# Performance work log

Hardware: AMD Instinct MI355X
Metric: run time of the kernel (lower is better)

The kernel has to match this reference:

```python
import jax, jax.numpy as jnp
import numpy as np

N, D_IN, D_OUT, E = 16384, 2048, 2048, 8


def setup_inputs() -> dict:
    key = jax.random.key(0)
    k1, k2, k3, k4 = jax.random.split(key, 4)
    x = jax.random.normal(k1, (N, D_IN), dtype=jnp.float32)
    idxs = jax.random.randint(k2, (N,), 0, E, dtype=jnp.int64)
    # nn.Linear params: weight [out, in], bias [out]; stacked over experts.
    W = jax.random.normal(k3, (E, D_OUT, D_IN), dtype=jnp.float32) * (1.0 / np.sqrt(D_IN))
    b = jax.random.normal(k4, (E, D_OUT), dtype=jnp.float32) * 0.01
    return {"x": x, "idxs": idxs, "W": W, "b": b}


def reference(x, idxs, W, b):
    # Hard-routed MoE: each token goes to exactly one expert's Linear, then ReLU.
    # Loop over the small fixed expert count; each iteration is one dense GEMM
    # over all tokens, combined with a per-token routing mask (equivalent math
    # to the original masked gather/scatter since every token matches exactly
    # one expert id in [0, E)).
    n_experts = W.shape[0]
    y = jnp.zeros((x.shape[0], W.shape[1]), dtype=x.dtype)
    for e in range(n_experts):
        mask = (idxs == e)[:, None]  # [N, 1]
        y_e = x @ W[e].T + b[e]      # [N, out]
        y = jnp.where(mask, y_e, y)
    return jax.nn.relu(y)
```

## Files before the change

### kernel.cpp

```cpp
#include <hip/hip_runtime.h>
#include <stdint.h>

#define N_TOK 16384
#define D_IN  2048
#define D_OUT 2048
#define NEXP  8

#define BM 256
#define BN 256
#define BK 32
#define NKT (D_IN / BK)

typedef __attribute__((ext_vector_type(8))) short bf16x8;
typedef __attribute__((ext_vector_type(4))) float f32x4;
typedef __attribute__((ext_vector_type(4))) unsigned short u16x4;

static __device__ __forceinline__ unsigned short f2bf(float x) {
  unsigned u = __builtin_bit_cast(unsigned, x);
  u += 0x7FFFu + ((u >> 16) & 1u);
  return (unsigned short)(u >> 16);
}
static __device__ __forceinline__ float bf2f(unsigned short h) {
  unsigned u = ((unsigned)h) << 16;
  return __builtin_bit_cast(float, u);
}

__global__ void zero_cnt(int* cnt) {
  if (threadIdx.x < NEXP) cnt[threadIdx.x] = 0;
}

__global__ void route_kernel(const int* __restrict__ idxs, int* __restrict__ cnt,
                             int* __restrict__ bucket) {
  __shared__ int hist[NEXP];
  __shared__ int base[NEXP];
  __shared__ int pos[NEXP];
  const int t = blockIdx.x * 256 + threadIdx.x;
  if (threadIdx.x < NEXP) { hist[threadIdx.x] = 0; pos[threadIdx.x] = 0; }
  __syncthreads();
  const int e = idxs[t];
  atomicAdd(&hist[e], 1);
  __syncthreads();
  if (threadIdx.x < NEXP)
    base[threadIdx.x] = atomicAdd(&cnt[threadIdx.x], hist[threadIdx.x]);
  __syncthreads();
  const int r = atomicAdd(&pos[e], 1);
  bucket[e * N_TOK + base[e] + r] = t;
}

__global__ void split_kernel(const float* __restrict__ in, unsigned short* __restrict__ hi,
                             unsigned short* __restrict__ lo, int n4) {
  int i = blockIdx.x * blockDim.x + threadIdx.x;
  int stride = gridDim.x * blockDim.x;
  const float4* in4 = (const float4*)in;
  for (; i < n4; i += stride) {
    float4 v = in4[i];
    float f[4] = {v.x, v.y, v.z, v.w};
    u16x4 h, l;
#pragma unroll
    for (int j = 0; j < 4; ++j) {
      unsigned short hh = f2bf(f[j]);
      h[j] = hh;
      l[j] = f2bf(f[j] - bf2f(hh));
    }
    *(u16x4*)(hi + (size_t)i * 4) = h;
    *(u16x4*)(lo + (size_t)i * 4) = l;
  }
}

#define GLD16(g, l)                                                                    \
  __builtin_amdgcn_global_load_lds((const __attribute__((address_space(1))) void*)(g), \
                                   (__attribute__((address_space(3))) void*)(l), 16, 0, 0)
#define SB() __builtin_amdgcn_sched_barrier(0)
#define BAR() __builtin_amdgcn_s_barrier()

template <int MH>
static __device__ __forceinline__ void loadA(const char* rb, int wr, int off0,
                                             bf16x8 (&afr)[4][2]) {
#pragma unroll
  for (int mf = 0; mf < 4; ++mf) {
    const int ro = (wr * 128 + MH * 64 + mf * 16) * 128;
    afr[mf][0] = *(const bf16x8*)(rb + ro + off0);
    afr[mf][1] = *(const bf16x8*)(rb + ro + (off0 ^ 64));
  }
}

template <int NH>
static __device__ __forceinline__ void loadB(const char* rb, int wc, int off0,
                                             bf16x8 (&bfr)[2][2]) {
#pragma unroll
  for (int nf = 0; nf < 2; ++nf) {
    const int ro = 32768 + (wc * 64 + NH * 32 + nf * 16) * 128;
    bfr[nf][0] = *(const bf16x8*)(rb + ro + off0);
    bfr[nf][1] = *(const bf16x8*)(rb + ro + (off0 ^ 64));
  }
}

template <int MH, int NH>
static __device__ __forceinline__ void mfma24(bf16x8 (&afr)[4][2], bf16x8 (&bfr)[2][2],
                                              f32x4 (&acc)[8][4]) {
#pragma unroll
  for (int mf = 0; mf < 4; ++mf)
#pragma unroll
    for (int nf = 0; nf < 2; ++nf) {
      f32x4 a = acc[MH * 4 + mf][NH * 2 + nf];
      a = __builtin_amdgcn_mfma_f32_16x16x32_bf16(afr[mf][0], bfr[nf][0], a, 0, 0, 0);
      a = __builtin_amdgcn_mfma_f32_16x16x32_bf16(afr[mf][0], bfr[nf][1], a, 0, 0, 0);
      a = __builtin_amdgcn_mfma_f32_16x16x32_bf16(afr[mf][1], bfr[nf][0], a, 0, 0, 0);
      acc[MH * 4 + mf][NH * 2 + nf] = a;
    }
}

__global__ __launch_bounds__(512, 2)
void moe_gemm(const unsigned short* __restrict__ xhi, const unsigned short* __restrict__ xlo,
              const unsigned short* __restrict__ whi, const unsigned short* __restrict__ wlo,
              const float* __restrict__ bias, const int* __restrict__ cnt,
              const int* __restrict__ bucket, float* __restrict__ out) {
  const int e = blockIdx.z;
  const int count = cnt[e];
  const int m0 = blockIdx.y * BM;
  if (m0 >= count) return;
  const int n0 = blockIdx.x * BN;

  __shared__ __align__(16) char sbuf[2][65536];
  __shared__ int rowtok[BM];

  const int tid = threadIdx.x;
  const int lane = tid & 63;
  const int w = tid >> 6;
  const int wr = w >> 2;
  const int wc = w & 3;

  if (tid < BM) {
    int r = m0 + tid;
    rowtok[tid] = bucket[e * N_TOK + (r < count ? r : count - 1)];
  }
  __syncthreads();

  const unsigned short* whiE = whi + (size_t)e * D_OUT * D_IN;
  const unsigned short* wloE = wlo + (size_t)e * D_OUT * D_IN;
  const unsigned short* srcb[8];
#pragma unroll
  for (int q = 0; q < 8; ++q) {
    const int r = (q & 3) * 64 + (tid >> 3);
    const int c = (tid & 7) ^ ((tid >> 3) & 7);
    const int half = c >> 2, kc = c & 3;
    if (q < 4) {
      const int tok = rowtok[r];
      srcb[q] = (half ? xlo : xhi) + (size_t)tok * D_IN + kc * 8;
    } else {
      srcb[q] = (half ? wloE : whiE) + (size_t)(n0 + r) * D_IN + kc * 8;
    }
  }
  const int dstoff = w * 1024;

  const int off0 = (lane & 15) * 128 + (((lane >> 4) ^ (lane & 7)) * 16);

  f32x4 acc[8][4];
#pragma unroll
  for (int i = 0; i < 8; ++i)
#pragma unroll
    for (int j = 0; j < 4; ++j) acc[i][j] = (f32x4)0.0f;
  bf16x8 afr[4][2], bfr[2][2];

  {
    char* wb = sbuf[0];
#pragma unroll
    for (int q = 0; q < 8; ++q) GLD16(srcb[q], wb + q * 8192 + dstoff);
  }
  asm volatile("s_waitcnt vmcnt(0)" ::: "memory");
  SB(); BAR(); SB();

  int cur = 0;
  for (int i = 0; i < NKT; ++i) {
    const char* rb = sbuf[cur];
    char* wb = sbuf[cur ^ 1];
    const int ktn = (i + 1) * BK;
    const bool nx = (i + 1 < NKT);

    loadA<0>(rb, wr, off0, afr);
    loadB<0>(rb, wc, off0, bfr);
    if (nx) { GLD16(srcb[0] + ktn, wb + 0 * 8192 + dstoff); GLD16(srcb[1] + ktn, wb + 1 * 8192 + dstoff); }
    SB(); BAR(); SB();
    __builtin_amdgcn_s_setprio(1); mfma24<0, 0>(afr, bfr, acc); __builtin_amdgcn_s_setprio(0);
    SB(); BAR(); SB();

    loadB<1>(rb, wc, off0, bfr);
    if (nx) { GLD16(srcb[2] + ktn, wb + 2 * 8192 + dstoff); GLD16(srcb[3] + ktn, wb + 3 * 8192 + dstoff); }
    SB(); BAR(); SB();
    __builtin_amdgcn_s_setprio(1); mfma24<0, 1>(afr, bfr, acc); __builtin_amdgcn_s_setprio(0);
    SB(); BAR(); SB();

    loadA<1>(rb, wr, off0, afr);
    loadB<0>(rb, wc, off0, bfr);
    if (nx) { GLD16(srcb[4] + ktn, wb + 4 * 8192 + dstoff); GLD16(srcb[5] + ktn, wb + 5 * 8192 + dstoff); }
    SB(); BAR(); SB();
    __builtin_amdgcn_s_setprio(1); mfma24<1, 0>(afr, bfr, acc); __builtin_amdgcn_s_setprio(0);
    SB(); BAR(); SB();

    loadB<1>(rb, wc, off0, bfr);
    if (nx) { GLD16(srcb[6] + ktn, wb + 6 * 8192 + dstoff); GLD16(srcb[7] + ktn, wb + 7 * 8192 + dstoff); }
    SB(); BAR(); SB();
    __builtin_amdgcn_s_setprio(1); mfma24<1, 1>(afr, bfr, acc); __builtin_amdgcn_s_setprio(0);
    asm volatile("s_waitcnt vmcnt(0)" ::: "memory");
    SB(); BAR(); SB();
    cur ^= 1;
  }

  const int r16 = lane & 15;
  const int rb4 = (lane >> 4) * 4;
#pragma unroll
  for (int n = 0; n < 4; ++n) {
    const int gn = n0 + wc * 64 + n * 16 + r16;
    const float bv = bias[e * D_OUT + gn];
#pragma unroll
    for (int m = 0; m < 8; ++m) {
      const int lr = wr * 128 + m * 16 + rb4;
#pragma unroll
      for (int i2 = 0; i2 < 4; ++i2) {
        const int row = lr + i2;
        if (m0 + row < count) {
          out[(size_t)rowtok[row] * D_OUT + gn] = fmaxf(acc[m][n][i2] + bv, 0.0f);
        }
      }
    }
  }
}

__global__ void fallback_kernel(const float* __restrict__ x, const int* __restrict__ idxs,
                                const float* __restrict__ W, const float* __restrict__ b,
                                float* __restrict__ out) {
  const int row = blockIdx.y;
  const int col = blockIdx.x * 256 + threadIdx.x;
  const int e = idxs[row];
  const float4* xr = (const float4*)(x + (size_t)row * D_IN);
  const float4* wr = (const float4*)(W + ((size_t)e * D_OUT + col) * D_IN);
  float acc = 0.f;
  for (int k = 0; k < D_IN / 4; ++k) {
    float4 a = xr[k], w = wr[k];
    acc += a.x * w.x + a.y * w.y + a.z * w.z + a.w * w.w;
  }
  out[(size_t)row * D_OUT + col] = fmaxf(acc + b[e * D_OUT + col], 0.0f);
}

extern "C" void kernel_launch(void* const* d_in, const int* in_sizes, int n_in,
                              void* d_out, int out_size, void* d_ws, size_t ws_size,
                              hipStream_t stream) {
  const float* x = (const float*)d_in[0];
  const int* idxs = (const int*)d_in[1];
  const float* W = (const float*)d_in[2];
  const float* b = (const float*)d_in[3];
  float* out = (float*)d_out;

  size_t off = 0;
  auto alloc = [&](size_t bytes) {
    void* p = (char*)d_ws + off;
    off += (bytes + 255) & ~(size_t)255;
    return p;
  };
  int* cnt = (int*)alloc(NEXP * sizeof(int));
  int* bucket = (int*)alloc((size_t)NEXP * N_TOK * sizeof(int));
  unsigned short* xhi = (unsigned short*)alloc((size_t)N_TOK * D_IN * 2);
  unsigned short* xlo = (unsigned short*)alloc((size_t)N_TOK * D_IN * 2);
  unsigned short* whi = (unsigned short*)alloc((size_t)NEXP * D_OUT * D_IN * 2);
  unsigned short* wlo = (unsigned short*)alloc((size_t)NEXP * D_OUT * D_IN * 2);

  if (off > ws_size) {
    dim3 g(D_OUT / 256, N_TOK, 1);
    fallback_kernel<<<g, 256, 0, stream>>>(x, idxs, W, b, out);
    return;
  }

  zero_cnt<<<1, 64, 0, stream>>>(cnt);
  route_kernel<<<N_TOK / 256, 256, 0, stream>>>(idxs, cnt, bucket);

  const int n4x = N_TOK * D_IN / 4;
  const int n4w = NEXP * D_OUT * D_IN / 4;
  split_kernel<<<2048, 256, 0, stream>>>(x, xhi, xlo, n4x);
  split_kernel<<<2048, 256, 0, stream>>>(W, whi, wlo, n4w);

  dim3 grid(D_OUT / BN, N_TOK / BM, NEXP);
  moe_gemm<<<grid, 512, 0, stream>>>(xhi, xlo, whi, wlo, b, cnt, bucket, out);
}
```

Baseline: 847.2 us.

## Restructure MoE GEMM to 256x128 tiles with triple-buffered LDS pipeline

```diff
diff --git a/kernel.cpp b/kernel.cpp
--- a/kernel.cpp
+++ b/kernel.cpp
@@ -7,9 +7,11 @@
 #define NEXP  8
 
 #define BM 256
-#define BN 256
+#define BN 128
 #define BK 32
 #define NKT (D_IN / BK)
+#define NX4 (N_TOK * D_IN / 4)
+#define NW4 (NEXP * D_OUT * D_IN / 4)
 
 typedef __attribute__((ext_vector_type(8))) short bf16x8;
 typedef __attribute__((ext_vector_type(4))) float f32x4;
@@ -47,23 +49,26 @@
   bucket[e * N_TOK + base[e] + r] = t;
 }
 
-__global__ void split_kernel(const float* __restrict__ in, unsigned short* __restrict__ hi,
-                             unsigned short* __restrict__ lo, int n4) {
-  int i = blockIdx.x * blockDim.x + threadIdx.x;
-  int stride = gridDim.x * blockDim.x;
-  const float4* in4 = (const float4*)in;
-  for (; i < n4; i += stride) {
-    float4 v = in4[i];
+__global__ void split_both(const float* __restrict__ x, const float* __restrict__ W,
+                           unsigned short* __restrict__ xhi, unsigned short* __restrict__ xlo,
+                           unsigned short* __restrict__ whi, unsigned short* __restrict__ wlo) {
+  const int total = NX4 + NW4;
+  for (int i = blockIdx.x * blockDim.x + threadIdx.x; i < total; i += gridDim.x * blockDim.x) {
+    const bool isx = (i < NX4);
+    const int j = isx ? i : i - NX4;
+    const float4 v = isx ? ((const float4*)x)[j] : ((const float4*)W)[j];
     float f[4] = {v.x, v.y, v.z, v.w};
     u16x4 h, l;
 #pragma unroll
-    for (int j = 0; j < 4; ++j) {
-      unsigned short hh = f2bf(f[j]);
-      h[j] = hh;
-      l[j] = f2bf(f[j] - bf2f(hh));
-    }
-    *(u16x4*)(hi + (size_t)i * 4) = h;
-    *(u16x4*)(lo + (size_t)i * 4) = l;
+    for (int k = 0; k < 4; ++k) {
+      unsigned short hh = f2bf(f[k]);
+      h[k] = hh;
+      l[k] = f2bf(f[k] - bf2f(hh));
+    }
+    unsigned short* dh = (isx ? xhi : whi) + (size_t)j * 4;
+    unsigned short* dl = (isx ? xlo : wlo) + (size_t)j * 4;
+    *(u16x4*)dh = h;
+    *(u16x4*)dl = l;
   }
 }
 
@@ -73,62 +78,29 @@
 #define SB() __builtin_amdgcn_sched_barrier(0)
 #define BAR() __builtin_amdgcn_s_barrier()
 
-template <int MH>
-static __device__ __forceinline__ void loadA(const char* rb, int wr, int off0,
-                                             bf16x8 (&afr)[4][2]) {
-#pragma unroll
-  for (int mf = 0; mf < 4; ++mf) {
-    const int ro = (wr * 128 + MH * 64 + mf * 16) * 128;
-    afr[mf][0] = *(const bf16x8*)(rb + ro + off0);
-    afr[mf][1] = *(const bf16x8*)(rb + ro + (off0 ^ 64));
-  }
-}
-
-template <int NH>
-static __device__ __forceinline__ void loadB(const char* rb, int wc, int off0,
-                                             bf16x8 (&bfr)[2][2]) {
-#pragma unroll
-  for (int nf = 0; nf < 2; ++nf) {
-    const int ro = 32768 + (wc * 64 + NH * 32 + nf * 16) * 128;
-    bfr[nf][0] = *(const bf16x8*)(rb + ro + off0);
-    bfr[nf][1] = *(const bf16x8*)(rb + ro + (off0 ^ 64));
-  }
-}
-
-template <int MH, int NH>
-static __device__ __forceinline__ void mfma24(bf16x8 (&afr)[4][2], bf16x8 (&bfr)[2][2],
-                                              f32x4 (&acc)[8][4]) {
-#pragma unroll
-  for (int mf = 0; mf < 4; ++mf)
-#pragma unroll
-    for (int nf = 0; nf < 2; ++nf) {
-      f32x4 a = acc[MH * 4 + mf][NH * 2 + nf];
-      a = __builtin_amdgcn_mfma_f32_16x16x32_bf16(afr[mf][0], bfr[nf][0], a, 0, 0, 0);
-      a = __builtin_amdgcn_mfma_f32_16x16x32_bf16(afr[mf][0], bfr[nf][1], a, 0, 0, 0);
-      a = __builtin_amdgcn_mfma_f32_16x16x32_bf16(afr[mf][1], bfr[nf][0], a, 0, 0, 0);
-      acc[MH * 4 + mf][NH * 2 + nf] = a;
-    }
-}
-
-__global__ __launch_bounds__(512, 2)
+__global__ __launch_bounds__(512)
 void moe_gemm(const unsigned short* __restrict__ xhi, const unsigned short* __restrict__ xlo,
               const unsigned short* __restrict__ whi, const unsigned short* __restrict__ wlo,
               const float* __restrict__ bias, const int* __restrict__ cnt,
               const int* __restrict__ bucket, float* __restrict__ out) {
-  const int e = blockIdx.z;
+  const int bid = blockIdx.x;
+  const int e = bid & 7;
+  const int rem = bid >> 3;
+  const int my = rem >> 4;
+  const int nb = rem & 15;
   const int count = cnt[e];
-  const int m0 = blockIdx.y * BM;
+  const int m0 = my * BM;
   if (m0 >= count) return;
-  const int n0 = blockIdx.x * BN;
-
-  __shared__ __align__(16) char sbuf[2][65536];
+  const int n0 = nb * BN;
+
+  __shared__ __align__(16) char sbuf[3][49152];
   __shared__ int rowtok[BM];
 
   const int tid = threadIdx.x;
   const int lane = tid & 63;
   const int w = tid >> 6;
-  const int wr = w >> 2;
-  const int wc = w & 3;
+  const int wrM = (w >> 1) * 64;
+  const int wcN = (w & 1) * 64;
 
   if (tid < BM) {
     int r = m0 + tid;
@@ -138,83 +110,105 @@
 
   const unsigned short* whiE = whi + (size_t)e * D_OUT * D_IN;
   const unsigned short* wloE = wlo + (size_t)e * D_OUT * D_IN;
-  const unsigned short* srcb[8];
-#pragma unroll
-  for (int q = 0; q < 8; ++q) {
-    const int r = (q & 3) * 64 + (tid >> 3);
-    const int c = (tid & 7) ^ ((tid >> 3) & 7);
+  const unsigned short* srcb[6];
+  {
+    const int g = tid >> 3;
+    const int c = (tid & 7) ^ (g & 7);
     const int half = c >> 2, kc = c & 3;
-    if (q < 4) {
-      const int tok = rowtok[r];
+#pragma unroll
+    for (int q = 0; q < 4; ++q) {
+      const int tok = rowtok[q * 64 + g];
       srcb[q] = (half ? xlo : xhi) + (size_t)tok * D_IN + kc * 8;
-    } else {
-      srcb[q] = (half ? wloE : whiE) + (size_t)(n0 + r) * D_IN + kc * 8;
-    }
-  }
-  const int dstoff = w * 1024;
+    }
+#pragma unroll
+    for (int q = 0; q < 2; ++q) {
+      srcb[4 + q] = (half ? wloE : whiE) + (size_t)(n0 + q * 64 + g) * D_IN + kc * 8;
+    }
+  }
+  const int dstw = w * 1024;
 
   const int off0 = (lane & 15) * 128 + (((lane >> 4) ^ (lane & 7)) * 16);
 
-  f32x4 acc[8][4];
-#pragma unroll
-  for (int i = 0; i < 8; ++i)
+  f32x4 acc[4][4];
+#pragma unroll
+  for (int i = 0; i < 4; ++i)
 #pragma unroll
     for (int j = 0; j < 4; ++j) acc[i][j] = (f32x4)0.0f;
-  bf16x8 afr[4][2], bfr[2][2];
-
+
+#pragma unroll
+  for (int q = 0; q < 4; ++q) GLD16(srcb[q], sbuf[0] + q * 8192 + dstw);
+#pragma unroll
+  for (int q = 0; q < 2; ++q) GLD16(srcb[4 + q], sbuf[0] + 32768 + q * 8192 + dstw);
+#pragma unroll
+  for (int q = 0; q < 4; ++q) GLD16(srcb[q] + BK, sbuf[1] + q * 8192 + dstw);
+#pragma unroll
+  for (int q = 0; q < 2; ++q) GLD16(srcb[4 + q] + BK, sbuf[1] + 32768 + q * 8192 + dstw);
+  SB();
+  asm volatile("s_waitcnt vmcnt(6)" ::: "memory");
+  BAR(); SB();
+
+#define COMPUTE(rb)                                                              \
+  {                                                                              \
+    bf16x8 ah[4], al[4], bh[4], bl[4];                                           \
+    _Pragma("unroll") for (int m = 0; m < 4; ++m) {                              \
+      const char* p = (rb) + (wrM + m * 16) * 128;                               \
+      ah[m] = *(const bf16x8*)(p + off0);                                        \
+      al[m] = *(const bf16x8*)(p + (off0 ^ 64));                                 \
+    }                                                                            \
+    _Pragma("unroll") for (int n = 0; n < 4; ++n) {                              \
+      const char* p = (rb) + 32768 + (wcN + n * 16) * 128;                       \
+      bh[n] = *(const bf16x8*)(p + off0);                                        \
+      bl[n] = *(const bf16x8*)(p + (off0 ^ 64));                                 \
+    }                                                                            \
+    __builtin_amdgcn_s_setprio(1);                                               \
+    _Pragma("unroll") for (int m = 0; m < 4; ++m)                                \
+    _Pragma("unroll") for (int n = 0; n < 4; ++n) {                              \
+      f32x4 a = acc[m][n];                                                       \
+      a = __builtin_amdgcn_mfma_f32_16x16x32_bf16(ah[m], bh[n], a, 0, 0, 0);     \
+      a = __builtin_amdgcn_mfma_f32_16x16x32_bf16(ah[m], bl[n], a, 0, 0, 0);     \
+      a = __builtin_amdgcn_mfma_f32_16x16x32_bf16(al[m], bh[n], a, 0, 0, 0);     \
+      acc[m][n] = a;                                                             \
+    }                                                                            \
+    __builtin_amdgcn_s_setprio(0);                                               \
+  }
+
+  int i = 0;
+  for (; i < NKT - 2; ++i) {
+    const char* rb = sbuf[i % 3];
+    char* wb = sbuf[(i + 2) % 3];
+    const int kt = (i + 2) * BK;
+#pragma unroll
+    for (int q = 0; q < 4; ++q) GLD16(srcb[q] + kt, wb + q * 8192 + dstw);
+#pragma unroll
+    for (int q = 0; q < 2; ++q) GLD16(srcb[4 + q] + kt, wb + 32768 + q * 8192 + dstw);
+    SB();
+    COMPUTE(rb);
+    SB();
+    asm volatile("s_waitcnt vmcnt(6)" ::: "memory");
+    BAR(); SB();
+  }
   {
-    char* wb = sbuf[0];
-#pragma unroll
-    for (int q = 0; q < 8; ++q) GLD16(srcb[q], wb + q * 8192 + dstoff);
-  }
-  asm volatile("s_waitcnt vmcnt(0)" ::: "memory");
-  SB(); BAR(); SB();
-
-  int cur = 0;
-  for (int i = 0; i < NKT; ++i) {
-    const char* rb = sbuf[cur];
-    char* wb = sbuf[cur ^ 1];
-    const int ktn = (i + 1) * BK;
-    const bool nx = (i + 1 < NKT);
-
-    loadA<0>(rb, wr, off0, afr);
-    loadB<0>(rb, wc, off0, bfr);
-    if (nx) { GLD16(srcb[0] + ktn, wb + 0 * 8192 + dstoff); GLD16(srcb[1] + ktn, wb + 1 * 8192 + dstoff); }
-    SB(); BAR(); SB();
-    __builtin_amdgcn_s_setprio(1); mfma24<0, 0>(afr, bfr, acc); __builtin_amdgcn_s_setprio(0);
-    SB(); BAR(); SB();
-
-    loadB<1>(rb, wc, off0, bfr);
-    if (nx) { GLD16(srcb[2] + ktn, wb + 2 * 8192 + dstoff); GLD16(srcb[3] + ktn, wb + 3 * 8192 + dstoff); }
-    SB(); BAR(); SB();
-    __builtin_amdgcn_s_setprio(1); mfma24<0, 1>(afr, bfr, acc); __builtin_amdgcn_s_setprio(0);
-    SB(); BAR(); SB();
-
-    loadA<1>(rb, wr, off0, afr);
-    loadB<0>(rb, wc, off0, bfr);
-    if (nx) { GLD16(srcb[4] + ktn, wb + 4 * 8192 + dstoff); GLD16(srcb[5] + ktn, wb + 5 * 8192 + dstoff); }
-    SB(); BAR(); SB();
-    __builtin_amdgcn_s_setprio(1); mfma24<1, 0>(afr, bfr, acc); __builtin_amdgcn_s_setprio(0);
-    SB(); BAR(); SB();
-
-    loadB<1>(rb, wc, off0, bfr);
-    if (nx) { GLD16(srcb[6] + ktn, wb + 6 * 8192 + dstoff); GLD16(srcb[7] + ktn, wb + 7 * 8192 + dstoff); }
-    SB(); BAR(); SB();
-    __builtin_amdgcn_s_setprio(1); mfma24<1, 1>(afr, bfr, acc); __builtin_amdgcn_s_setprio(0);
+    const char* rb = sbuf[i % 3];
+    COMPUTE(rb);
+    SB();
     asm volatile("s_waitcnt vmcnt(0)" ::: "memory");
-    SB(); BAR(); SB();
-    cur ^= 1;
+    BAR(); SB();
+    ++i;
+  }
+  {
+    const char* rb = sbuf[i % 3];
+    COMPUTE(rb);
   }
 
   const int r16 = lane & 15;
   const int rb4 = (lane >> 4) * 4;
 #pragma unroll
   for (int n = 0; n < 4; ++n) {
-    const int gn = n0 + wc * 64 + n * 16 + r16;
+    const int gn = n0 + wcN + n * 16 + r16;
     const float bv = bias[e * D_OUT + gn];
 #pragma unroll
-    for (int m = 0; m < 8; ++m) {
-      const int lr = wr * 128 + m * 16 + rb4;
+    for (int m = 0; m < 4; ++m) {
+      const int lr = wrM + m * 16 + rb4;
 #pragma unroll
       for (int i2 = 0; i2 < 4; ++i2) {
         const int row = lr + i2;
@@ -224,6 +218,7 @@
       }
     }
   }
+#undef COMPUTE
 }
 
 __global__ void fallback_kernel(const float* __restrict__ x, const int* __restrict__ idxs,
@@ -272,12 +267,8 @@
 
   zero_cnt<<<1, 64, 0, stream>>>(cnt);
   route_kernel<<<N_TOK / 256, 256, 0, stream>>>(idxs, cnt, bucket);
-
-  const int n4x = N_TOK * D_IN / 4;
-  const int n4w = NEXP * D_OUT * D_IN / 4;
-  split_kernel<<<2048, 256, 0, stream>>>(x, xhi, xlo, n4x);
-  split_kernel<<<2048, 256, 0, stream>>>(W, whi, wlo, n4w);
-
-  dim3 grid(D_OUT / BN, N_TOK / BM, NEXP);
-  moe_gemm<<<grid, 512, 0, stream>>>(xhi, xlo, whi, wlo, b, cnt, bucket, out);
-}
+  split_both<<<2048, 256, 0, stream>>>(x, W, xhi, xlo, whi, wlo);
+
+  const int nblk = NEXP * (N_TOK / BM) * (D_OUT / BN);
+  moe_gemm<<<nblk, 512, 0, stream>>>(xhi, xlo, whi, wlo, b, cnt, bucket, out);
+}
```

After: 953.6 us. 1.13x slower.
